# Performance work log

Hardware: AMD Instinct MI355X
Metric: run time of the kernel (lower is better)

The kernel has to match this reference:

```python
import jax, jax.numpy as jnp
import numpy as np

S, B, D, H = 1024, 8, 1024, 8  # seq, batch, model_dim, num_heads


def setup_inputs() -> dict:
    key = jax.random.key(0)
    ks = jax.random.split(key, 5)
    scale = 1.0 / np.sqrt(D)
    x = jax.random.normal(ks[0], (S, B, D), dtype=jnp.float32)
    # per-head PyTorch MHA params: in_proj_weight (3D, D), in_proj_bias (3D,),
    # out_proj weight (D, D), bias (D,)
    w_in = jax.random.normal(ks[1], (H, 3 * D, D), dtype=jnp.float32) * scale
    b_in = jax.random.normal(ks[2], (H, 3 * D), dtype=jnp.float32) * 0.02
    w_out = jax.random.normal(ks[3], (H, D, D), dtype=jnp.float32) * scale
    b_out = jax.random.normal(ks[4], (H, D), dtype=jnp.float32) * 0.02
    return {"x": x, "w_in": w_in, "b_in": b_in, "w_out": w_out, "b_out": b_out}


def reference(x, w_in, b_in, w_out, b_out):
    d = x.shape[-1]
    scale = 1.0 / jnp.sqrt(jnp.asarray(d, dtype=x.dtype))
    # split in_proj into q/k/v pieces: each [H, D, D] (PyTorch applies x @ W.T + b)
    wq, wk, wv = w_in[:, :d], w_in[:, d:2 * d], w_in[:, 2 * d:]
    bq, bk, bv = b_in[:, :d], b_in[:, d:2 * d], b_in[:, 2 * d:]
    # projections, head-batched: [H, S, B, D]
    q = jnp.einsum('sbd,hed->hsbe', x, wq) + bq[:, None, None, :]
    k = jnp.einsum('sbd,hed->hsbe', x, wk) + bk[:, None, None, :]
    v = jnp.einsum('sbd,hed->hsbe', x, wv) + bv[:, None, None, :]
    # scaled dot-product attention, full-width single head per module
    scores = jnp.einsum('hsbe,htbe->hbst', q * scale, k)  # [H, B, S, S]
    attn = jax.nn.softmax(scores, axis=-1)
    o = jnp.einsum('hbst,htbe->hsbe', attn, v)  # [H, S, B, D]
    out_h = jnp.einsum('hsbe,hfe->hsbf', o, w_out) + b_out[:, None, None, :]
    return out_h.sum(axis=0)  # [S, B, D]
```

## Files before the change

kernel.cpp:

```cpp
#include <hip/hip_runtime.h>
#include <hip/hip_bf16.h>


typedef __attribute__((ext_vector_type(8))) __bf16 bf16x8;
typedef __attribute__((ext_vector_type(4))) float f32x4;

__device__ __forceinline__ unsigned short f2bf(float f) {
  union { float f; unsigned u; } x; x.f = f;
  unsigned r = x.u + 0x7fffu + ((x.u >> 16) & 1u);
  return (unsigned short)(r >> 16);
}
__device__ __forceinline__ float bf2f(unsigned short u) {
  union { unsigned u; float f; } x; x.u = ((unsigned)u) << 16;
  return x.f;
}

__device__ __forceinline__ void gload16(const void* g, void* l) {
  __builtin_amdgcn_global_load_lds(
      (const __attribute__((address_space(1))) void*)g,
      (__attribute__((address_space(3))) void*)l, 16, 0, 0);
}

#define SBAR()  do { __builtin_amdgcn_sched_barrier(0); __builtin_amdgcn_s_barrier(); \
                     __builtin_amdgcn_sched_barrier(0); } while (0)
#define LGKM0() do { asm volatile("s_waitcnt lgkmcnt(0)" ::: "memory"); \
                     __builtin_amdgcn_sched_barrier(0); } while (0)
#define VMC4()  do { asm volatile("s_waitcnt vmcnt(4)" ::: "memory"); \
                     __builtin_amdgcn_sched_barrier(0); } while (0)

struct Frags { bf16x8 aF[4][2]; bf16x8 b0F[2][2]; bf16x8 b1F[2][2]; };

template<int QUAD>
__device__ __forceinline__ void qreads(const char* sm, int bb, int aRow, int bRow,
                                       int kx0, int kx1, Frags& fr)
{
  if constexpr (QUAD == 0) {
#pragma unroll
    for (int m = 0; m < 4; ++m) {
      fr.aF[m][0] = *(const bf16x8*)(sm + bb + aRow + m * 2048 + kx0);
      fr.aF[m][1] = *(const bf16x8*)(sm + bb + aRow + m * 2048 + kx1);
    }
#pragma unroll
    for (int n = 0; n < 2; ++n) {
      fr.b0F[n][0] = *(const bf16x8*)(sm + bb + bRow + n * 2048 + kx0);
      fr.b0F[n][1] = *(const bf16x8*)(sm + bb + bRow + n * 2048 + kx1);
    }
  } else if constexpr (QUAD == 1) {
#pragma unroll
    for (int n = 0; n < 2; ++n) {
      fr.b1F[n][0] = *(const bf16x8*)(sm + bb + bRow + (2 + n) * 2048 + kx0);
      fr.b1F[n][1] = *(const bf16x8*)(sm + bb + bRow + (2 + n) * 2048 + kx1);
    }
  } else if constexpr (QUAD == 2) {
#pragma unroll
    for (int m = 0; m < 4; ++m) {
      fr.aF[m][0] = *(const bf16x8*)(sm + bb + aRow + (4 + m) * 2048 + kx0);
      fr.aF[m][1] = *(const bf16x8*)(sm + bb + aRow + (4 + m) * 2048 + kx1);
    }
  }
}

template<int QUAD>
__device__ __forceinline__ void qmfma(f32x4 acc[8][4], Frags& fr)
{
  constexpr int mo = (QUAD >= 2) ? 4 : 0;
  constexpr int no = (QUAD == 1 || QUAD == 2) ? 2 : 0;
  __builtin_amdgcn_s_setprio(1);
#pragma unroll
  for (int m = 0; m < 4; ++m)
#pragma unroll
    for (int n = 0; n < 2; ++n)
#pragma unroll
      for (int ks = 0; ks < 2; ++ks) {
        const bf16x8 bv = (no == 0) ? fr.b0F[n][ks] : fr.b1F[n][ks];
        acc[mo + m][no + n] =
            __builtin_amdgcn_mfma_f32_16x16x32_bf16(fr.aF[m][ks], bv, acc[mo + m][no + n], 0, 0, 0);
      }
  __builtin_amdgcn_s_setprio(0);
  __builtin_amdgcn_sched_barrier(0);
}

template<int EPI, int NT_FAST>
__global__ __launch_bounds__(512, 1)
void gemm256_nt(const unsigned short* __restrict__ A,
                const unsigned short* __restrict__ B,
                void* __restrict__ C,
                const float* __restrict__ bias,
                float alpha, int K,
                long lda, long ldb, long ldc,
                long offA_h, long offA_b,
                long offB_h, long offB_b,
                long offC_h, long offC_b,
                long offBias_h, long offBias_b,
                int MT, int NTt, int nb)
{
  __shared__ __align__(16) char sm[131072];

  const int nwg = gridDim.x;
  const int swz = (blockIdx.x & 7) * (nwg >> 3) + (blockIdx.x >> 3);
  const int per_z = MT * NTt;
  const int z = swz / per_z;
  const int r = swz - z * per_z;
  const int mt = NT_FAST ? (r / NTt) : (r % MT);
  const int nt = NT_FAST ? (r % NTt) : (r / MT);
  const int h = z / nb, bz = z - h * nb;

  const unsigned short* Ablk = A + h * offA_h + bz * offA_b + (long)mt * 256 * lda;
  const unsigned short* Bblk = B + h * offB_h + bz * offB_b + (long)nt * 256 * ldb;

  const int tid  = threadIdx.x;
  const int lane = tid & 63;
  const int w    = tid >> 6;
  const int wr   = w >> 2, wc = w & 3;

  const int rA  = tid >> 3;
  const int cSw = (tid ^ (tid >> 3)) & 7;

  const int aRow = wr * 16384 + (lane & 15) * 128;
  const int bRow = 32768 + (wc >> 1) * 16384 + ((wc & 1) * 64 + (lane & 15)) * 128;
  const int kq = (lane >> 4) * 16, sw = (lane & 7) << 4;
  const int kx0 = kq ^ sw;
  const int kx1 = (64 + kq) ^ sw;

  const int NT = K >> 6;
  const int NIT = NT >> 1;

  f32x4 acc[8][4] = {};
  Frags fr;

  auto stageA = [&](int half, int kt, int region) {
    const unsigned short* g = Ablk + ((long)(half * 128) + rA) * lda + (long)kt * 64 + cSw * 8;
    gload16(g,            sm + region + tid * 16);
    gload16(g + 64 * lda, sm + region + 8192 + tid * 16);
  };
  auto stageB = [&](int half, int kt, int region) {
    const unsigned short* g = Bblk + ((long)(half * 128) + rA) * ldb + (long)kt * 64 + cSw * 8;
    gload16(g,            sm + region + tid * 16);
    gload16(g + 64 * ldb, sm + region + 8192 + tid * 16);
  };

  stageA(0, 0, 0);
  stageA(1, 0, 16384);
  stageB(0, 0, 32768);
  stageB(1, 0, 49152);
  stageB(0, 1, 65536 + 32768);
  stageB(1, 1, 65536 + 49152);
  VMC4();
  SBAR();

#pragma unroll 1
  for (int it = 0; it < NIT; ++it) {
    const int kt1 = 2 * it + 1;
    const int kt2a = 2 * it + 2, kt2 = kt2a < NT ? kt2a : NT - 1;
    const int kt3a = 2 * it + 3, kt3 = kt3a < NT ? kt3a : NT - 1;

    qreads<0>(sm, 0, aRow, bRow, kx0, kx1, fr);
    stageA(0, kt1, 65536);
    SBAR(); LGKM0(); qmfma<0>(acc, fr); SBAR();

    qreads<1>(sm, 0, aRow, bRow, kx0, kx1, fr);
    stageA(1, kt1, 65536 + 16384);
    SBAR(); LGKM0(); qmfma<1>(acc, fr); SBAR();

    qreads<2>(sm, 0, aRow, bRow, kx0, kx1, fr);
    stageB(0, kt2, 32768);
    SBAR(); LGKM0(); qmfma<2>(acc, fr); SBAR();

    stageB(1, kt2, 49152);
    SBAR(); LGKM0(); qmfma<3>(acc, fr);
    VMC4();
    SBAR();

    qreads<0>(sm, 65536, aRow, bRow, kx0, kx1, fr);
    stageA(0, kt2, 0);
    SBAR(); LGKM0(); qmfma<0>(acc, fr); SBAR();

    qreads<1>(sm, 65536, aRow, bRow, kx0, kx1, fr);
    stageA(1, kt2, 16384);
    SBAR(); LGKM0(); qmfma<1>(acc, fr); SBAR();

    qreads<2>(sm, 65536, aRow, bRow, kx0, kx1, fr);
    stageB(0, kt3, 65536 + 32768);
    SBAR(); LGKM0(); qmfma<2>(acc, fr); SBAR();

    stageB(1, kt3, 65536 + 49152);
    SBAR(); LGKM0(); qmfma<3>(acc, fr);
    VMC4();
    SBAR();
  }

  const long crow0 = (long)mt * 256 + wr * 128;
  const long ccol0 = (long)nt * 256 + wc * 64;
  const long cbase = h * offC_h + bz * offC_b;
  const float* bptr = bias ? (bias + h * offBias_h + bz * offBias_b) : nullptr;

  float rp[8][4];

#pragma unroll
  for (int m = 0; m < 8; ++m) {
    float rv4[4];
    if constexpr (EPI == 4) {
#pragma unroll
      for (int j = 0; j < 4; ++j)
        rv4[j] = 1.0f / bptr[crow0 + m * 16 + (lane >> 4) * 4 + j];
    }
#pragma unroll
    for (int n = 0; n < 4; ++n) {
      const long col = ccol0 + n * 16 + (lane & 15);
      const float cb = (EPI == 1) ? bptr[col] : 0.0f;
#pragma unroll
      for (int j = 0; j < 4; ++j) {
        const long row = crow0 + m * 16 + (lane >> 4) * 4 + j;
        float v = acc[m][n][j] * alpha;
        if constexpr (EPI == 1) v += cb;
        if constexpr (EPI == 2) v += bptr[row];
        if constexpr (EPI == 3) v = __expf(v);
        if constexpr (EPI == 4) v *= rv4[j];
        const long idx = cbase + row * ldc + col;
        if constexpr (EPI == 0) {
          ((float*)C)[idx] = v;
        } else {
          const unsigned short hb = f2bf(v);
          ((unsigned short*)C)[idx] = hb;
          if constexpr (EPI == 3) {
            const float vr = bf2f(hb);
            rp[m][j] = (n == 0) ? vr : rp[m][j] + vr;
          }
        }
      }
    }
  }

  if constexpr (EPI == 3) {
#pragma unroll
    for (int m = 0; m < 8; ++m)
#pragma unroll
      for (int j = 0; j < 4; ++j) {
        float s = rp[m][j];
        s += __shfl_xor(s, 1); s += __shfl_xor(s, 2);
        s += __shfl_xor(s, 4); s += __shfl_xor(s, 8);
        if ((lane & 15) == 0) {
          const long row = crow0 + m * 16 + (lane >> 4) * 4 + j;
          atomicAdd((float*)&bptr[row], s);
        }
      }
  }
}

__global__ __launch_bounds__(256)
void conv_x(const float* __restrict__ in, unsigned short* __restrict__ out)
{
  const long i = (long)blockIdx.x * 256 + threadIdx.x;
  const long o = i << 2;
  const long b = o >> 20, rem = o & 1048575;
  const long s = rem >> 10, d = rem & 1023;
  const float4 v = *(const float4*)(in + s * 8192 + b * 1024 + d);
  ushort4 u; u.x = f2bf(v.x); u.y = f2bf(v.y); u.z = f2bf(v.z); u.w = f2bf(v.w);
  *(ushort4*)(out + o) = u;
}

__global__ __launch_bounds__(256)
void conv_bf16(const float* __restrict__ in, unsigned short* __restrict__ out, long n4)
{
  const long i = (long)blockIdx.x * 256 + threadIdx.x;
  if (i >= n4) return;
  const float4 v = ((const float4*)in)[i];
  ushort4 o; o.x = f2bf(v.x); o.y = f2bf(v.y); o.z = f2bf(v.z); o.w = f2bf(v.w);
  ((ushort4*)out)[i] = o;
}

__global__ __launch_bounds__(256)
void conv_wout(const float* __restrict__ in, unsigned short* __restrict__ out)
{
  const long i = (long)blockIdx.x * 256 + threadIdx.x;
  const long o = i << 2;
  const long f = o >> 13, r = o & 8191;
  const long h = r >> 10, e = r & 1023;
  const float4 v = *(const float4*)(in + h * 1048576 + f * 1024 + e);
  ushort4 u; u.x = f2bf(v.x); u.y = f2bf(v.y); u.z = f2bf(v.z); u.w = f2bf(v.w);
  *(ushort4*)(out + o) = u;
}

__global__ __launch_bounds__(256)
void bias_sum_k(const float* __restrict__ b_out, float* __restrict__ bsum)
{
  const int f = blockIdx.x * 256 + threadIdx.x;
  if (f < 1024) {
    float s = 0.f;
#pragma unroll
    for (int h = 0; h < 8; ++h) s += b_out[h * 1024 + f];
    bsum[f] = s;
  }
}

__global__ __launch_bounds__(256)
void zero_k(float* __restrict__ p, long n4)
{
  const long i = (long)blockIdx.x * 256 + threadIdx.x;
  if (i < n4) ((float4*)p)[i] = make_float4(0.f, 0.f, 0.f, 0.f);
}

__global__ __launch_bounds__(256)
void add_out_k(const float* __restrict__ p, float* __restrict__ out,
               const float* __restrict__ bsum)
{
  const long i = (long)blockIdx.x * 256 + threadIdx.x;
  const float4 a = ((const float4*)p)[i];
  const float4 b = ((const float4*)(p + 8388608))[i];
  const float4 s = ((const float4*)bsum)[i & 255];
  float4 o;
  o.x = a.x + b.x + s.x; o.y = a.y + b.y + s.y;
  o.z = a.z + b.z + s.z; o.w = a.w + b.w + s.w;
  ((float4*)out)[i] = o;
}

extern "C" void kernel_launch(void* const* d_in, const int* in_sizes, int n_in,
                              void* d_out, int out_size, void* d_ws, size_t ws_size,
                              hipStream_t stream)
{
  const float* x     = (const float*)d_in[0];
  const float* w_in  = (const float*)d_in[1];
  const float* b_in  = (const float*)d_in[2];
  const float* w_out = (const float*)d_in[3];
  const float* b_out = (const float*)d_in[4];
  float* out = (float*)d_out;

  char* ws = (char*)d_ws;
  const long MB = 1ll << 20;
  unsigned short* Xr    = (unsigned short*)(ws);
  unsigned short* Wob   = (unsigned short*)(ws + 16 * MB);
  float*          bsum  = (float*)         (ws + 32 * MB);
  unsigned short* WbAll = (unsigned short*)(ws + 33 * MB);
  unsigned short* Ocat  = (unsigned short*)(ws + 81 * MB);
  unsigned short* QKg   = (unsigned short*)(ws + 209 * MB);
  unsigned short* E     = (unsigned short*)(ws + 273 * MB);
  unsigned short* VT    = (unsigned short*)(ws + 305 * MB);
  float*          rsum  = (float*)         (ws + 337 * MB);
  float*          Opart = (float*)QKg;

  dim3 blk(256), blk512(512);

  conv_x    <<<8192,  blk, 0, stream>>>(x, Xr);
  conv_bf16 <<<24576, blk, 0, stream>>>(w_in, WbAll, 6291456);
  conv_wout <<<8192,  blk, 0, stream>>>(w_out, Wob);
  bias_sum_k<<<4,     blk, 0, stream>>>(b_out, bsum);
  zero_k    <<<64,    blk, 0, stream>>>(rsum, 16384);

  for (int g = 0; g < 4; ++g) {
    const long gW = (long)g * 6291456;
    const long gB = (long)g * 6144;
    float* rs = rsum + (long)g * 16384;

    gemm256_nt<1,0><<<512, blk512, 0, stream>>>(
        Xr, WbAll + gW, QKg, b_in + gB, 1.0f, 1024,
        1024, 1024, 4096,  0, 0,  3145728, 0,  2048, 0,  3072, 0,  32, 8, 1);

    gemm256_nt<2,0><<<256, blk512, 0, stream>>>(
        WbAll + gW + 2097152, Xr, VT, b_in + gB + 2048, 1.0f, 1024,
        1024, 1024, 1024,  3145728, 0,  0, 1048576,  8388608, 1048576,  3072, 0,  4, 4, 8);

    gemm256_nt<3,0><<<256, blk512, 0, stream>>>(
        QKg, QKg + 1024, E, rs, 0.03125f, 1024,
        4096, 4096, 1024,  2048, 4194304,  2048, 4194304,  8388608, 1048576,  8192, 1024,  4, 4, 8);

    gemm256_nt<4,0><<<256, blk512, 0, stream>>>(
        E, VT, Ocat + (long)g * 2048, rs, 1.0f, 1024,
        1024, 1024, 65536,  8388608, 1048576,  8388608, 1048576,  1024, 8192,  8192, 1024,  4, 4, 8);
  }

  gemm256_nt<0,1><<<256, blk512, 0, stream>>>(
      Ocat, Wob, Opart, nullptr, 1.0f, 4096,
      8192, 8192, 1024,  0, 4096,  0, 4096,  0, 8388608,  0, 0,  32, 4, 2);

  add_out_k<<<8192, blk, 0, stream>>>(Opart, out, bsum);
}
```

Measured before the change: 950.4 us.

## Issue all LDS fragment reads upfront and use partial lgkmcnt waits

Restructures the GEMM main loop so each half-iteration issues all A and B fragment LDS reads at once into separate register sets (adding an aG buffer for the second A half). It then overlaps MFMA quads with outstanding reads through partial lgkmcnt waits instead of full waits. Barriers per half-iteration drop from eight to two, and global prefetch issue is regrouped. This raises register pressure and relies on correct counting of outstanding LDS ops and on the staging order avoiding overwrites of data still being read.

Result: slower. 1.216 ms (+27.9%).

```diff
diff --git a/kernel.cpp b/kernel.cpp
--- a/kernel.cpp
+++ b/kernel.cpp
@@ -21,42 +21,47 @@
       (__attribute__((address_space(3))) void*)l, 16, 0, 0);
 }
 
-#define SBAR()  do { __builtin_amdgcn_sched_barrier(0); __builtin_amdgcn_s_barrier(); \
-                     __builtin_amdgcn_sched_barrier(0); } while (0)
-#define LGKM0() do { asm volatile("s_waitcnt lgkmcnt(0)" ::: "memory"); \
-                     __builtin_amdgcn_sched_barrier(0); } while (0)
-#define VMC4()  do { asm volatile("s_waitcnt vmcnt(4)" ::: "memory"); \
-                     __builtin_amdgcn_sched_barrier(0); } while (0)
-
-struct Frags { bf16x8 aF[4][2]; bf16x8 b0F[2][2]; bf16x8 b1F[2][2]; };
-
-template<int QUAD>
-__device__ __forceinline__ void qreads(const char* sm, int bb, int aRow, int bRow,
-                                       int kx0, int kx1, Frags& fr)
-{
-  if constexpr (QUAD == 0) {
-#pragma unroll
-    for (int m = 0; m < 4; ++m) {
-      fr.aF[m][0] = *(const bf16x8*)(sm + bb + aRow + m * 2048 + kx0);
-      fr.aF[m][1] = *(const bf16x8*)(sm + bb + aRow + m * 2048 + kx1);
-    }
-#pragma unroll
-    for (int n = 0; n < 2; ++n) {
-      fr.b0F[n][0] = *(const bf16x8*)(sm + bb + bRow + n * 2048 + kx0);
-      fr.b0F[n][1] = *(const bf16x8*)(sm + bb + bRow + n * 2048 + kx1);
-    }
-  } else if constexpr (QUAD == 1) {
-#pragma unroll
-    for (int n = 0; n < 2; ++n) {
-      fr.b1F[n][0] = *(const bf16x8*)(sm + bb + bRow + (2 + n) * 2048 + kx0);
-      fr.b1F[n][1] = *(const bf16x8*)(sm + bb + bRow + (2 + n) * 2048 + kx1);
-    }
-  } else if constexpr (QUAD == 2) {
-#pragma unroll
-    for (int m = 0; m < 4; ++m) {
-      fr.aF[m][0] = *(const bf16x8*)(sm + bb + aRow + (4 + m) * 2048 + kx0);
-      fr.aF[m][1] = *(const bf16x8*)(sm + bb + aRow + (4 + m) * 2048 + kx1);
-    }
+#define SB()    __builtin_amdgcn_sched_barrier(0)
+#define SBAR()  do { SB(); __builtin_amdgcn_s_barrier(); SB(); } while (0)
+#define LGKMC(n) do { asm volatile("s_waitcnt lgkmcnt(" #n ")" ::: "memory"); SB(); } while (0)
+#define VMC4()  do { asm volatile("s_waitcnt vmcnt(4)" ::: "memory"); SB(); } while (0)
+
+struct Frags { bf16x8 aF[4][2]; bf16x8 aG[4][2]; bf16x8 b0F[2][2]; bf16x8 b1F[2][2]; };
+
+__device__ __forceinline__ void qrA0(const char* sm, int bb, int aRow,
+                                     int kx0, int kx1, Frags& fr)
+{
+#pragma unroll
+  for (int m = 0; m < 4; ++m) {
+    fr.aF[m][0] = *(const bf16x8*)(sm + bb + aRow + m * 2048 + kx0);
+    fr.aF[m][1] = *(const bf16x8*)(sm + bb + aRow + m * 2048 + kx1);
+  }
+}
+__device__ __forceinline__ void qrB0(const char* sm, int bb, int bRow,
+                                     int kx0, int kx1, Frags& fr)
+{
+#pragma unroll
+  for (int n = 0; n < 2; ++n) {
+    fr.b0F[n][0] = *(const bf16x8*)(sm + bb + bRow + n * 2048 + kx0);
+    fr.b0F[n][1] = *(const bf16x8*)(sm + bb + bRow + n * 2048 + kx1);
+  }
+}
+__device__ __forceinline__ void qrB1(const char* sm, int bb, int bRow,
+                                     int kx0, int kx1, Frags& fr)
+{
+#pragma unroll
+  for (int n = 0; n < 2; ++n) {
+    fr.b1F[n][0] = *(const bf16x8*)(sm + bb + bRow + (2 + n) * 2048 + kx0);
+    fr.b1F[n][1] = *(const bf16x8*)(sm + bb + bRow + (2 + n) * 2048 + kx1);
+  }
+}
+__device__ __forceinline__ void qrA1(const char* sm, int bb, int aRow,
+                                     int kx0, int kx1, Frags& fr)
+{
+#pragma unroll
+  for (int m = 0; m < 4; ++m) {
+    fr.aG[m][0] = *(const bf16x8*)(sm + bb + aRow + (4 + m) * 2048 + kx0);
+    fr.aG[m][1] = *(const bf16x8*)(sm + bb + aRow + (4 + m) * 2048 + kx1);
   }
 }
 
@@ -72,12 +77,13 @@
     for (int n = 0; n < 2; ++n)
 #pragma unroll
       for (int ks = 0; ks < 2; ++ks) {
+        const bf16x8 av = (QUAD >= 2) ? fr.aG[m][ks] : fr.aF[m][ks];
         const bf16x8 bv = (no == 0) ? fr.b0F[n][ks] : fr.b1F[n][ks];
         acc[mo + m][no + n] =
-            __builtin_amdgcn_mfma_f32_16x16x32_bf16(fr.aF[m][ks], bv, acc[mo + m][no + n], 0, 0, 0);
+            __builtin_amdgcn_mfma_f32_16x16x32_bf16(av, bv, acc[mo + m][no + n], 0, 0, 0);
       }
   __builtin_amdgcn_s_setprio(0);
-  __builtin_amdgcn_sched_barrier(0);
+  SB();
 }
 
 template<int EPI, int NT_FAST>
@@ -139,6 +145,23 @@
     gload16(g + 64 * ldb, sm + region + 8192 + tid * 16);
   };
 
+  auto group = [&](int bb, int oth, int ktA, int ktB) {
+    qrA0(sm, bb, aRow, kx0, kx1, fr);
+    qrB0(sm, bb, bRow, kx0, kx1, fr); SB();
+    qrB1(sm, bb, bRow, kx0, kx1, fr); SB();
+    qrA1(sm, bb, aRow, kx0, kx1, fr); SB();
+    stageA(0, ktA, oth);
+    stageA(1, ktA, oth + 16384);
+    LGKMC(12); qmfma<0>(acc, fr);
+    LGKMC(8);  qmfma<1>(acc, fr);
+    SBAR();
+    stageB(0, ktB, bb + 32768);
+    stageB(1, ktB, bb + 49152);
+    LGKMC(0);  qmfma<2>(acc, fr); qmfma<3>(acc, fr);
+    VMC4();
+    SBAR();
+  };
+
   stageA(0, 0, 0);
   stageA(1, 0, 16384);
   stageB(0, 0, 32768);
@@ -154,39 +177,8 @@
     const int kt2a = 2 * it + 2, kt2 = kt2a < NT ? kt2a : NT - 1;
     const int kt3a = 2 * it + 3, kt3 = kt3a < NT ? kt3a : NT - 1;
 
-    qreads<0>(sm, 0, aRow, bRow, kx0, kx1, fr);
-    stageA(0, kt1, 65536);
-    SBAR(); LGKM0(); qmfma<0>(acc, fr); SBAR();
-
-    qreads<1>(sm, 0, aRow, bRow, kx0, kx1, fr);
-    stageA(1, kt1, 65536 + 16384);
-    SBAR(); LGKM0(); qmfma<1>(acc, fr); SBAR();
-
-    qreads<2>(sm, 0, aRow, bRow, kx0, kx1, fr);
-    stageB(0, kt2, 32768);
-    SBAR(); LGKM0(); qmfma<2>(acc, fr); SBAR();
-
-    stageB(1, kt2, 49152);
-    SBAR(); LGKM0(); qmfma<3>(acc, fr);
-    VMC4();
-    SBAR();
-
-    qreads<0>(sm, 65536, aRow, bRow, kx0, kx1, fr);
-    stageA(0, kt2, 0);
-    SBAR(); LGKM0(); qmfma<0>(acc, fr); SBAR();
-
-    qreads<1>(sm, 65536, aRow, bRow, kx0, kx1, fr);
-    stageA(1, kt2, 16384);
-    SBAR(); LGKM0(); qmfma<1>(acc, fr); SBAR();
-
-    qreads<2>(sm, 65536, aRow, bRow, kx0, kx1, fr);
-    stageB(0, kt3, 65536 + 32768);
-    SBAR(); LGKM0(); qmfma<2>(acc, fr); SBAR();
-
-    stageB(1, kt3, 65536 + 49152);
-    SBAR(); LGKM0(); qmfma<3>(acc, fr);
-    VMC4();
-    SBAR();
+    group(0,     65536, kt1, kt2);
+    group(65536, 0,     kt2, kt3);
   }
 
   const long crow0 = (long)mt * 256 + wr * 128;
```
